# Performance work log

Measured on AMD Instinct MI355X. Metric: run time of the kernel, lower is better.

## Reference

```python
import jax, jax.numpy as jnp
import numpy as np

N, K, C, G = 100000, 16, 64, 8
EPS = 1e-5


def bn(x, gamma, beta):
    # training-mode BatchNorm1d over all dims except channel (last)
    axes = tuple(range(x.ndim - 1))
    m = jnp.mean(x, axis=axes)
    v = jnp.var(x, axis=axes)
    return (x - m) * jax.lax.rsqrt(v + EPS) * gamma + beta


def setup_inputs() -> dict:
    key = jax.random.key(0)
    ks = jax.random.split(key, 16)

    def lin(k, i, o):
        return (jax.random.normal(k, (i, o), jnp.float32) / np.sqrt(i)).astype(jnp.float32)

    feat = jax.random.normal(ks[0], (N, C), jnp.float32)
    coord = jax.random.uniform(ks[1], (N, 3), jnp.float32) * 10.0
    ref = jax.random.randint(ks[2], (N, K), 0, N)
    drop = jax.random.uniform(ks[3], (N, K)) < 0.05  # some padded (-1) neighbors
    ref = jnp.where(drop, -1, ref)

    return {
        "feat": feat, "coord": coord, "reference_index": ref,
        "wq": lin(ks[4], C, C), "bq": jnp.zeros((C,), jnp.float32),
        "gq": jnp.ones((C,), jnp.float32), "betaq": jnp.zeros((C,), jnp.float32),
        "wk": lin(ks[5], C, C), "bk": jnp.zeros((C,), jnp.float32),
        "gk": jnp.ones((C,), jnp.float32), "betak": jnp.zeros((C,), jnp.float32),
        "wv": lin(ks[6], C, C), "bv": jnp.zeros((C,), jnp.float32),
        "wp1": lin(ks[7], 3, C), "bp1": jnp.zeros((C,), jnp.float32),
        "gp": jnp.ones((C,), jnp.float32), "betap": jnp.zeros((C,), jnp.float32),
        "wp2": lin(ks[8], C, C), "bp2": jnp.zeros((C,), jnp.float32),
        "ww1": lin(ks[9], C, G), "bw1": jnp.zeros((G,), jnp.float32),
        "gw": jnp.ones((G,), jnp.float32), "betaw": jnp.zeros((G,), jnp.float32),
        "ww2": lin(ks[10], G, G), "bw2": jnp.zeros((G,), jnp.float32),
    }


def reference(feat, coord, reference_index,
              wq, bq, gq, betaq,
              wk, bk, gk, betak,
              wv, bv,
              wp1, bp1, gp, betap,
              wp2, bp2,
              ww1, bw1, gw, betaw,
              ww2, bw2):
    # q/k/v projections
    q = jax.nn.relu(bn(feat @ wq + bq, gq, betaq))   # [N, C]
    k = jax.nn.relu(bn(feat @ wk + bk, gk, betak))   # [N, C]
    v = feat @ wv + bv                                # [N, C]

    idx = jnp.clip(reference_index, 0, N - 1)         # clipped gather index [N, K]
    mask = (reference_index >= 0).astype(feat.dtype)  # sign(ref + 1)

    key_n = k[idx]                                    # [N, K, C] neighbor keys
    val = v[idx]                                      # [N, K, C]
    pos = coord[idx] - coord[:, None, :]              # [N, K, 3] relative coords

    relation_qk = key_n - q[:, None, :]               # [N, K, C]

    # pe_bias branch
    peb = jax.nn.relu(bn(pos @ wp1 + bp1, gp, betap)) @ wp2 + bp2  # [N, K, C]
    relation_qk = relation_qk + peb
    val = val + peb

    # weight encoding -> grouped softmax over neighbors, masked
    w = jax.nn.relu(bn(relation_qk @ ww1 + bw1, gw, betaw)) @ ww2 + bw2  # [N, K, G]
    w = jax.nn.softmax(w, axis=1) * mask[:, :, None]

    val = val.reshape(N, K, G, C // G)
    out = jnp.einsum('nsgi,nsg->ngi', val, w).reshape(N, C)
    return out
```

## Files before the change

### kernel.cpp

```cpp
#include <hip/hip_runtime.h>
#include <hip/hip_bf16.h>

#define NPTS 100000
#define KNBR 16
#define CCH  64
#define GRP  8
#define BN_EPS 1e-5f
#define NROW (NPTS * KNBR)
#define NBATCH (NROW / 64)
#define NPB   ((NPTS + 63) / 64)

#define O_QLINH 0
#define O_KLINH (NPTS * 32)
#define O_VLINH (NPTS * 64)
#define O_STAT  (NPTS * 96)
#define O_AFF   (O_STAT + 416)
#define O_W2W1  (O_AFF + 416)
#define O_BW1E  (O_W2W1 + 512)
#define O_QW1   (O_BW1E + 8)
#define O_KW1   (O_QW1 + NPTS * 8)

typedef __attribute__((ext_vector_type(8))) short short8;
typedef __attribute__((ext_vector_type(4))) short short4v;
typedef __attribute__((ext_vector_type(4))) float f32x4;
#define MFMA16(a, b, c) __builtin_amdgcn_mfma_f32_16x16x32_bf16(a, b, c, 0, 0, 0)

__device__ __forceinline__ int clip_idx(int r) {
    int i = r < 0 ? 0 : r;
    return i >= NPTS ? NPTS - 1 : i;
}
__device__ __forceinline__ unsigned short f2bf(float x) {
    union { float f; unsigned u; } v; v.f = x;
    unsigned r = v.u + 0x7fffu + ((v.u >> 16) & 1u);
    return (unsigned short)(r >> 16);
}
__device__ __forceinline__ float bf2f(unsigned short h) {
    union { unsigned u; float f; } v; v.u = ((unsigned)h) << 16;
    return v.f;
}
__device__ __forceinline__ int physK(int s) {
    return (s >> 5) * 32 + ((s >> 2) & 3) * 8 + ((s >> 4) & 1) * 4 + (s & 3);
}
__device__ __forceinline__ int aOff(int r, int p) {
    return r * 64 + (((p >> 3) ^ (r & 7)) << 3) + (p & 7);
}
__device__ __forceinline__ int kib_of(int i, int q) {
    return (i < 4) ? (4 * q + i) : (16 + 4 * q + (i - 4));
}

__global__ __launch_bounds__(512) void k_prep(
    const float* __restrict__ wp2, const float* __restrict__ ww1,
    const float* __restrict__ bw1, const float* __restrict__ bp2,
    float* __restrict__ stat, float* __restrict__ w2w1, float* __restrict__ bw1e)
{
    int t = threadIdx.x;
    if (t < 416) stat[t] = 0.f;
    int j = t >> 3, g = t & 7;
    float acc = 0.f;
    #pragma unroll 16
    for (int c = 0; c < 64; ++c) acc = fmaf(wp2[j * 64 + c], ww1[c * 8 + g], acc);
    w2w1[t] = acc;
    if (t < 8) {
        float b = bw1[t];
        #pragma unroll 16
        for (int c = 0; c < 64; ++c) b = fmaf(bp2[c], ww1[c * 8 + t], b);
        bw1e[t] = b;
    }
}

#define QKV_BLOCKS 512
__global__ __launch_bounds__(256) void k_qkv(
    const float* __restrict__ feat,
    const float* __restrict__ wq, const float* __restrict__ bq,
    const float* __restrict__ wk, const float* __restrict__ bk,
    const float* __restrict__ wv, const float* __restrict__ bv,
    const float* __restrict__ bp2,
    const float* __restrict__ coord, const int* __restrict__ ref,
    short* __restrict__ QlinH, short* __restrict__ KlinH, short* __restrict__ VlinH,
    float* __restrict__ stat)
{
    __shared__ short sA[4096];
    __shared__ float s_red[9];
    const int tid = threadIdx.x, lane = tid & 63, w = tid >> 6;
    const int q = lane >> 4, c15 = lane & 15;

    if (blockIdx.x >= QKV_BLOCKS) {
        float m[9];
        #pragma unroll
        for (int i = 0; i < 9; ++i) m[i] = 0.f;
        const int gid = (blockIdx.x - QKV_BLOCKS) * 256 + tid;
        const int stride = 128 * 256;
        for (int row = gid; row < NROW; row += stride) {
            int n = row >> 4;
            int idx = clip_idx(ref[row]);
            float px = coord[idx * 3 + 0] - coord[n * 3 + 0];
            float py = coord[idx * 3 + 1] - coord[n * 3 + 1];
            float pz = coord[idx * 3 + 2] - coord[n * 3 + 2];
            m[0] += px; m[1] += py; m[2] += pz;
            m[3] = fmaf(px, px, m[3]); m[4] = fmaf(py, py, m[4]); m[5] = fmaf(pz, pz, m[5]);
            m[6] = fmaf(px, py, m[6]); m[7] = fmaf(px, pz, m[7]); m[8] = fmaf(py, pz, m[8]);
        }
        if (tid < 9) s_red[tid] = 0.f;
        __syncthreads();
        #pragma unroll
        for (int off = 32; off >= 1; off >>= 1) {
            #pragma unroll
            for (int i = 0; i < 9; ++i) m[i] += __shfl_xor(m[i], off, 64);
        }
        if (lane == 0) {
            #pragma unroll
            for (int i = 0; i < 9; ++i) atomicAdd(&s_red[i], m[i]);
        }
        __syncthreads();
        if (tid < 9) atomicAdd(&stat[256 + tid], s_red[tid]);
        return;
    }

    short8 bfrag[3][2];
    float bias[3];
    #pragma unroll
    for (int t = 0; t < 3; ++t) {
        int gt = w * 3 + t;
        const float* W = (gt < 4) ? wq : (gt < 8) ? wk : wv;
        const float* B = (gt < 4) ? bq : (gt < 8) ? bk : bv;
        int col = (gt * 16 + c15) & 63;
        bias[t] = B[col] + (gt >= 8 ? bp2[col] : 0.f);
        #pragma unroll
        for (int kt = 0; kt < 2; ++kt) {
            short8 bb;
            #pragma unroll
            for (int i = 0; i < 8; ++i) {
                int kk = kt * 32 + kib_of(i, q);
                bb[i] = (short)f2bf(W[kk * 64 + col]);
            }
            bfrag[t][kt] = bb;
        }
    }
    float st_s[3], st_q[3];
    #pragma unroll
    for (int t = 0; t < 3; ++t) { st_s[t] = 0.f; st_q[t] = 0.f; }

    const int c4 = c15 * 4;
    const int pk4 = physK(c4);

    for (int b = blockIdx.x; b < NPB; b += QKV_BLOCKS) {
        const int pbase = b * 64;
        #pragma unroll
        for (int i = 0; i < 4; ++i) {
            int p = w * 16 + i * 4 + q;
            int n = pbase + p;
            float4 v = make_float4(0.f, 0.f, 0.f, 0.f);
            if (n < NPTS) v = *(const float4*)(feat + n * 64 + c4);
            short4v h;
            h[0] = (short)f2bf(v.x); h[1] = (short)f2bf(v.y);
            h[2] = (short)f2bf(v.z); h[3] = (short)f2bf(v.w);
            *(short4v*)(sA + aOff(p, pk4)) = h;
        }
        __syncthreads();
        #pragma unroll
        for (int mt = 0; mt < 4; ++mt) {
            int r = mt * 16 + c15;
            int ch0 = q ^ (r & 7);
            int ch1 = (4 + q) ^ (r & 7);
            short8 a0 = *(const short8*)(sA + r * 64 + (ch0 << 3));
            short8 a1 = *(const short8*)(sA + r * 64 + (ch1 << 3));
            #pragma unroll
            for (int t = 0; t < 3; ++t) {
                f32x4 acc = (f32x4){0.f, 0.f, 0.f, 0.f};
                acc = MFMA16(a0, bfrag[t][0], acc);
                acc = MFMA16(a1, bfrag[t][1], acc);
                int gt = w * 3 + t;
                #pragma unroll
                for (int rg = 0; rg < 4; ++rg) {
                    int row = mt * 16 + 4 * q + rg;
                    int n = pbase + row;
                    if (n < NPTS) {
                        unsigned short h = f2bf(acc[rg] + bias[t]);
                        float vr = bf2f(h);
                        if (gt < 4)      QlinH[n * 64 + gt * 16 + c15] = (short)h;
                        else if (gt < 8) KlinH[n * 64 + (gt - 4) * 16 + c15] = (short)h;
                        else             VlinH[n * 64 + (gt - 8) * 16 + c15] = (short)h;
                        if (gt < 8) { st_s[t] += vr; st_q[t] = fmaf(vr, vr, st_q[t]); }
                    }
                }
            }
        }
        __syncthreads();
    }
    #pragma unroll
    for (int t = 0; t < 3; ++t) {
        st_s[t] += __shfl_xor(st_s[t], 16, 64); st_s[t] += __shfl_xor(st_s[t], 32, 64);
        st_q[t] += __shfl_xor(st_q[t], 16, 64); st_q[t] += __shfl_xor(st_q[t], 32, 64);
    }
    if (q == 0) {
        #pragma unroll
        for (int t = 0; t < 3; ++t) {
            int gt = w * 3 + t;
            if (gt < 4) {
                atomicAdd(&stat[gt * 16 + c15], st_s[t]);
                atomicAdd(&stat[64 + gt * 16 + c15], st_q[t]);
            } else if (gt < 8) {
                atomicAdd(&stat[128 + (gt - 4) * 16 + c15], st_s[t]);
                atomicAdd(&stat[192 + (gt - 4) * 16 + c15], st_q[t]);
            }
        }
    }
}

__global__ __launch_bounds__(192) void k_finA(
    const float* __restrict__ gq, const float* __restrict__ betaq,
    const float* __restrict__ gk, const float* __restrict__ betak,
    const float* __restrict__ gp, const float* __restrict__ betap,
    const float* __restrict__ wp1, const float* __restrict__ bp1,
    const float* __restrict__ stat, float* __restrict__ aff)
{
    int t = threadIdx.x;
    if (t < 64) {
        float m = stat[t] / (float)NPTS;
        float v = stat[64 + t] / (float)NPTS - m * m;
        float a = gq[t] * rsqrtf(v + BN_EPS);
        aff[t] = a;
        aff[64 + t] = betaq[t] - m * a;
    } else if (t < 128) {
        int c = t - 64;
        float m = stat[128 + c] / (float)NPTS;
        float v = stat[192 + c] / (float)NPTS - m * m;
        float a = gk[c] * rsqrtf(v + BN_EPS);
        aff[128 + c] = a;
        aff[192 + c] = betak[c] - m * a;
    } else {
        int c = t - 128;
        const float R = (float)NROW;
        float Ex = stat[256] / R, Ey = stat[257] / R, Ez = stat[258] / R;
        float Exx = stat[259] / R, Eyy = stat[260] / R, Ezz = stat[261] / R;
        float Exy = stat[262] / R, Exz = stat[263] / R, Eyz = stat[264] / R;
        float Cxx = Exx - Ex * Ex, Cyy = Eyy - Ey * Ey, Czz = Ezz - Ez * Ez;
        float Cxy = Exy - Ex * Ey, Cxz = Exz - Ex * Ez, Cyz = Eyz - Ey * Ez;
        float a0 = wp1[c], a1 = wp1[64 + c], a2 = wp1[128 + c];
        float mean = a0 * Ex + a1 * Ey + a2 * Ez + bp1[c];
        float var = a0 * a0 * Cxx + a1 * a1 * Cyy + a2 * a2 * Czz
                  + 2.f * (a0 * a1 * Cxy + a0 * a2 * Cxz + a1 * a2 * Cyz);
        float a = gp[c] * rsqrtf(var + BN_EPS);
        aff[256 + c] = a;
        aff[320 + c] = betap[c] - mean * a;
    }
}

__global__ __launch_bounds__(128) void k_qkw(
    const short* __restrict__ QlinH, const short* __restrict__ KlinH,
    const float* __restrict__ ww1, const float* __restrict__ aff,
    float* __restrict__ QW1, float* __restrict__ KW1)
{
    __shared__ short sA[2][8192];
    const int tid = threadIdx.x, lane = tid & 63, w = tid >> 6;
    const int q = lane >> 4, g = lane & 15;
    short8 bimg[2];
    #pragma unroll
    for (int kt = 0; kt < 2; ++kt) {
        short8 bb;
        #pragma unroll
        for (int i = 0; i < 8; ++i) {
            int s = kt * 32 + kib_of(i, q);
            bb[i] = (short)f2bf(g < 8 ? ww1[s * 8 + g] : 0.f);
        }
        bimg[kt] = bb;
    }
    const int r8 = lane >> 3, c8 = (lane & 7) * 8;
    f32x4 qa0 = *(const f32x4*)(aff + c8),       qa1 = *(const f32x4*)(aff + c8 + 4);
    f32x4 qb0 = *(const f32x4*)(aff + 64 + c8),  qb1 = *(const f32x4*)(aff + 64 + c8 + 4);
    f32x4 ka0 = *(const f32x4*)(aff + 128 + c8), ka1 = *(const f32x4*)(aff + 128 + c8 + 4);
    f32x4 kb0 = *(const f32x4*)(aff + 192 + c8), kb1 = *(const f32x4*)(aff + 192 + c8 + 4);
    const int pkA = physK(c8), pkB = physK(c8 + 4);
    short* AQ = sA[w];
    short* AK = sA[w] + 4096;

    for (int b = blockIdx.x * 2 + w; b < NPB; b += gridDim.x * 2) {
        const int pbase = b * 64;
        #pragma unroll
        for (int it = 0; it < 8; ++it) {
            int p = it * 8 + r8;
            int n = pbase + p;
            short8 qraw = {0,0,0,0,0,0,0,0}, kraw = {0,0,0,0,0,0,0,0};
            if (n < NPTS) {
                qraw = *(const short8*)(QlinH + n * 64 + c8);
                kraw = *(const short8*)(KlinH + n * 64 + c8);
            }
            short4v qlo, qhi, klo, khi;
            #pragma unroll
            for (int e = 0; e < 4; ++e) {
                qlo[e] = (short)f2bf(fmaxf(fmaf(bf2f((unsigned short)qraw[e]), qa0[e], qb0[e]), 0.f));
                qhi[e] = (short)f2bf(fmaxf(fmaf(bf2f((unsigned short)qraw[e + 4]), qa1[e], qb1[e]), 0.f));
                klo[e] = (short)f2bf(fmaxf(fmaf(bf2f((unsigned short)kraw[e]), ka0[e], kb0[e]), 0.f));
                khi[e] = (short)f2bf(fmaxf(fmaf(bf2f((unsigned short)kraw[e + 4]), ka1[e], kb1[e]), 0.f));
            }
            *(short4v*)(AQ + aOff(p, pkA)) = qlo;
            *(short4v*)(AQ + aOff(p, pkB)) = qhi;
            *(short4v*)(AK + aOff(p, pkA)) = klo;
            *(short4v*)(AK + aOff(p, pkB)) = khi;
        }
        #pragma unroll
        for (int mt = 0; mt < 4; ++mt) {
            f32x4 aq = (f32x4){0.f, 0.f, 0.f, 0.f};
            f32x4 ak = (f32x4){0.f, 0.f, 0.f, 0.f};
            int r = mt * 16 + g;
            #pragma unroll
            for (int kt = 0; kt < 2; ++kt) {
                int chunk = (kt * 4 + q) ^ (r & 7);
                aq = MFMA16(*(const short8*)(AQ + r * 64 + (chunk << 3)), bimg[kt], aq);
                ak = MFMA16(*(const short8*)(AK + r * 64 + (chunk << 3)), bimg[kt], ak);
            }
            if (g < 8) {
                #pragma unroll
                for (int rg = 0; rg < 4; ++rg) {
                    int n = pbase + mt * 16 + 4 * q + rg;
                    if (n < NPTS) {
                        QW1[n * 8 + g] = aq[rg];
                        KW1[n * 8 + g] = ak[rg];
                    }
                }
            }
        }
    }
}

__global__ __launch_bounds__(128) void k_wstats(
    const float* __restrict__ coord, const int* __restrict__ ref,
    const float* __restrict__ wp1, const float* __restrict__ bp1,
    const float* __restrict__ bw1e, const float* __restrict__ w2w1,
    const float* __restrict__ QW1, const float* __restrict__ KW1,
    const float* __restrict__ aff, float* __restrict__ stat)
{
    __shared__ short sP[2][4096];
    __shared__ float sPos[2][256];
    __shared__ int   sIdx[2][64];
    __shared__ float sRed[16];
    const int tid = threadIdx.x, lane = tid & 63, w = tid >> 6;
    const int q = lane >> 4, g = lane & 15, g7 = lane & 7;
    short8 bimg[2];
    #pragma unroll
    for (int kt = 0; kt < 2; ++kt) {
        short8 bb;
        #pragma unroll
        for (int i = 0; i < 8; ++i) {
            int s = kt * 32 + kib_of(i, q);
            bb[i] = (short)f2bf(g < 8 ? w2w1[s * 8 + g] : 0.f);
        }
        bimg[kt] = bb;
    }
    if (tid < 16) sRed[tid] = 0.f;
    __syncthreads();

    const float pa = aff[256 + lane];
    const float A0 = pa * wp1[lane], A1 = pa * wp1[64 + lane], A2 = pa * wp1[128 + lane];
    const float B0 = fmaf(pa, bp1[lane], aff[320 + lane]);
    const float bwg = bw1e[g7];
    const int pk = physK(lane);

    short* P = sP[w];
    float* pos = sPos[w];
    int* idxs = sIdx[w];
    float accS = 0.f, accQ = 0.f;

    for (int b = blockIdx.x * 2 + w; b < NBATCH; b += gridDim.x * 2) {
        const int rbase = b * 64;
        const int p0 = b * 4;
        {
            int r = ref[rbase + lane];
            int idx = clip_idx(r);
            idxs[lane] = idx;
            int n = p0 + (lane >> 4);
            pos[lane * 4 + 0] = coord[idx * 3 + 0] - coord[n * 3 + 0];
            pos[lane * 4 + 1] = coord[idx * 3 + 1] - coord[n * 3 + 1];
            pos[lane * 4 + 2] = coord[idx * 3 + 2] - coord[n * 3 + 2];
        }
        float kwc[16], qwc[4];
        #pragma unroll
        for (int mt = 0; mt < 4; ++mt) {
            int4 i4 = *(const int4*)(idxs + mt * 16 + 4 * q);
            kwc[mt * 4 + 0] = KW1[i4.x * 8 + g7];
            kwc[mt * 4 + 1] = KW1[i4.y * 8 + g7];
            kwc[mt * 4 + 2] = KW1[i4.z * 8 + g7];
            kwc[mt * 4 + 3] = KW1[i4.w * 8 + g7];
            qwc[mt] = QW1[(p0 + mt) * 8 + g7];
        }
        #pragma unroll 8
        for (int rr = 0; rr < 64; ++rr) {
            f32x4 pp = *(const f32x4*)(pos + rr * 4);
            float p1v = fmaxf(fmaf(pp.x, A0, fmaf(pp.y, A1, fmaf(pp.z, A2, B0))), 0.f);
            P[aOff(rr, pk)] = (short)f2bf(p1v);
        }
        #pragma unroll
        for (int mt = 0; mt < 4; ++mt) {
            f32x4 acc = (f32x4){0.f, 0.f, 0.f, 0.f};
            int r = mt * 16 + g;
            #pragma unroll
            for (int kt = 0; kt < 2; ++kt) {
                int chunk = (kt * 4 + q) ^ (r & 7);
                acc = MFMA16(*(const short8*)(P + r * 64 + (chunk << 3)), bimg[kt], acc);
            }
            if (g < 8) {
                float dq = bwg - qwc[mt];
                #pragma unroll
                for (int rg = 0; rg < 4; ++rg) {
                    float W = acc[rg] + kwc[mt * 4 + rg] + dq;
                    accS += W;
                    accQ = fmaf(W, W, accQ);
                }
            }
        }
    }
    accS += __shfl_xor(accS, 16, 64); accS += __shfl_xor(accS, 32, 64);
    accQ += __shfl_xor(accQ, 16, 64); accQ += __shfl_xor(accQ, 32, 64);
    if (lane < 8) {
        atomicAdd(&sRed[lane], accS);
        atomicAdd(&sRed[8 + lane], accQ);
    }
    __syncthreads();
    if (tid < 16) atomicAdd(&stat[384 + tid], sRed[tid]);
}

__global__ __launch_bounds__(64) void k_finB(
    const float* __restrict__ gw_, const float* __restrict__ betaw,
    const float* __restrict__ stat, float* __restrict__ aff)
{
    int t = threadIdx.x;
    if (t < 8) {
        const float M = (float)NROW;
        float m = stat[384 + t] / M;
        float v = stat[392 + t] / M - m * m;
        float a = gw_[t] * rsqrtf(v + BN_EPS);
        aff[384 + t] = a;
        aff[392 + t] = betaw[t] - m * a;
    }
}

__global__ __launch_bounds__(128) void k_final(
    const float* __restrict__ coord, const int* __restrict__ ref,
    const float* __restrict__ wp1, const float* __restrict__ bp1,
    const float* __restrict__ wp2,
    const float* __restrict__ bw1e, const float* __restrict__ w2w1,
    const float* __restrict__ ww2, const float* __restrict__ bw2,
    const float* __restrict__ QW1, const float* __restrict__ KW1,
    const short* __restrict__ VlinH,
    const float* __restrict__ aff, float* __restrict__ out)
{
    __shared__ short sP[2][4096];
    __shared__ float sPos[2][256];
    __shared__ int   sIdx[2][64];
    __shared__ float sWn[2][576];
    __shared__ float sW2[72];
    const int tid = threadIdx.x, lane = tid & 63, w = tid >> 6;
    const int q = lane >> 4, g15 = lane & 15, g7 = lane & 7;

    if (tid < 64) sW2[tid] = ww2[tid];
    else if (tid < 72) sW2[tid] = bw2[tid - 64];
    __syncthreads();

    short8 bw_img[2];
    #pragma unroll
    for (int kt = 0; kt < 2; ++kt) {
        short8 bb;
        #pragma unroll
        for (int i = 0; i < 8; ++i) {
            int s = kt * 32 + kib_of(i, q);
            bb[i] = (short)f2bf(g15 < 8 ? w2w1[s * 8 + g15] : 0.f);
        }
        bw_img[kt] = bb;
    }
    short8 b1[8];
    #pragma unroll
    for (int tt = 0; tt < 8; ++tt) {
        int kt = tt & 1, nt = tt >> 1;
        short8 bb;
        #pragma unroll
        for (int i = 0; i < 8; ++i) {
            int kk = kt * 32 + kib_of(i, q);
            bb[i] = (short)f2bf(wp2[kk * 64 + nt * 16 + g15]);
        }
        b1[tt] = bb;
    }

    const float pa = aff[256 + lane];
    const float A0 = pa * wp1[lane], A1 = pa * wp1[64 + lane], A2 = pa * wp1[128 + lane];
    const float B0 = fmaf(pa, bp1[lane], aff[320 + lane]);
    const float bwg = bw1e[g7];
    const float wag = aff[384 + g7], wbg = aff[392 + g7];
    const int pk = physK(lane);

    short* P = sP[w];
    float* pos = sPos[w];
    int* idxs = sIdx[w];
    float* wn = sWn[w];

    for (int b = blockIdx.x * 2 + w; b < NBATCH; b += gridDim.x * 2) {
        const int rbase = b * 64;
        const int p0 = b * 4;
        {
            int r = ref[rbase + lane];
            int idx = clip_idx(r);
            idxs[lane] = idx;
            int n = p0 + (lane >> 4);
            pos[lane * 4 + 0] = coord[idx * 3 + 0] - coord[n * 3 + 0];
            pos[lane * 4 + 1] = coord[idx * 3 + 1] - coord[n * 3 + 1];
            pos[lane * 4 + 2] = coord[idx * 3 + 2] - coord[n * 3 + 2];
            pos[lane * 4 + 3] = (r >= 0) ? 1.f : 0.f;
        }
        float kwc[16], qwc[4];
        #pragma unroll
        for (int mt = 0; mt < 4; ++mt) {
            int4 i4 = *(const int4*)(idxs + mt * 16 + 4 * q);
            kwc[mt * 4 + 0] = KW1[i4.x * 8 + g7];
            kwc[mt * 4 + 1] = KW1[i4.y * 8 + g7];
            kwc[mt * 4 + 2] = KW1[i4.z * 8 + g7];
            kwc[mt * 4 + 3] = KW1[i4.w * 8 + g7];
            qwc[mt] = QW1[(p0 + mt) * 8 + g7];
        }
        #pragma unroll 8
        for (int rr = 0; rr < 64; ++rr) {
            f32x4 pp = *(const f32x4*)(pos + rr * 4);
            float p1v = fmaxf(fmaf(pp.x, A0, fmaf(pp.y, A1, fmaf(pp.z, A2, B0))), 0.f);
            P[aOff(rr, pk)] = (short)f2bf(p1v);
        }
        #pragma unroll
        for (int mt = 0; mt < 4; ++mt) {
            f32x4 acc = (f32x4){0.f, 0.f, 0.f, 0.f};
            int r = mt * 16 + g15;
            #pragma unroll
            for (int kt = 0; kt < 2; ++kt) {
                int chunk = (kt * 4 + q) ^ (r & 7);
                acc = MFMA16(*(const short8*)(P + r * 64 + (chunk << 3)), bw_img[kt], acc);
            }
            if (g15 < 8) {
                float dq = bwg - qwc[mt];
                #pragma unroll
                for (int rg = 0; rg < 4; ++rg) {
                    int row = mt * 16 + 4 * q + rg;
                    float W = acc[rg] + kwc[mt * 4 + rg] + dq;
                    wn[row * 9 + g15] = fmaxf(fmaf(wag, W, wbg), 0.f);
                }
            }
        }
        {
            float h[8];
            #pragma unroll
            for (int gg = 0; gg < 8; ++gg) h[gg] = wn[lane * 9 + gg];
            float mask = pos[lane * 4 + 3];
            #pragma unroll
            for (int o = 0; o < 8; ++o) {
                float acc = sW2[64 + o];
                #pragma unroll
                for (int gg = 0; gg < 8; ++gg) acc = fmaf(h[gg], sW2[gg * 8 + o], acc);
                float e = __expf(acc);
                float s = e;
                s += __shfl_xor(s, 1, 64);
                s += __shfl_xor(s, 2, 64);
                s += __shfl_xor(s, 4, 64);
                s += __shfl_xor(s, 8, 64);
                wn[lane * 9 + o] = e * __builtin_amdgcn_rcpf(s) * mask;
            }
        }
        #pragma unroll
        for (int mt = 0; mt < 4; ++mt) {
            int4 i4 = *(const int4*)(idxs + mt * 16 + 4 * q);
            int ia[4] = {i4.x, i4.y, i4.z, i4.w};
            unsigned short vc[16];
            #pragma unroll
            for (int rg = 0; rg < 4; ++rg) {
                const short* vb = VlinH + ia[rg] * 64 + g15;
                #pragma unroll
                for (int nt = 0; nt < 4; ++nt)
                    vc[rg * 4 + nt] = (unsigned short)vb[nt * 16];
            }
            int r = mt * 16 + g15;
            int c0 = q ^ (r & 7);
            int c1 = (4 + q) ^ (r & 7);
            short8 a0 = *(const short8*)(P + r * 64 + (c0 << 3));
            short8 a1 = *(const short8*)(P + r * 64 + (c1 << 3));
            const int ro0 = (mt * 16 + 4 * q) * 9;
            #pragma unroll
            for (int nt = 0; nt < 4; ++nt) {
                f32x4 acc = (f32x4){0.f, 0.f, 0.f, 0.f};
                acc = MFMA16(a0, b1[nt * 2 + 0], acc);
                acc = MFMA16(a1, b1[nt * 2 + 1], acc);
                int col = nt * 16 + g15;
                int o = nt * 2 + (g15 >> 3);
                float part = 0.f;
                #pragma unroll
                for (int rg = 0; rg < 4; ++rg) {
                    float v = bf2f(vc[rg * 4 + nt]);
                    part = fmaf(v + acc[rg], wn[ro0 + rg * 9 + o], part);
                }
                part += __shfl_xor(part, 16, 64);
                part += __shfl_xor(part, 32, 64);
                if (q == 0) out[(p0 + mt) * 64 + col] = part;
            }
        }
    }
}

extern "C" void kernel_launch(void* const* d_in, const int* in_sizes, int n_in,
                              void* d_out, int out_size, void* d_ws, size_t ws_size,
                              hipStream_t stream)
{
    const float* feat  = (const float*)d_in[0];
    const float* coord = (const float*)d_in[1];
    const int*   ref   = (const int*)d_in[2];
    const float* wq    = (const float*)d_in[3];
    const float* bq    = (const float*)d_in[4];
    const float* gq    = (const float*)d_in[5];
    const float* betaq = (const float*)d_in[6];
    const float* wk    = (const float*)d_in[7];
    const float* bk    = (const float*)d_in[8];
    const float* gk    = (const float*)d_in[9];
    const float* betak = (const float*)d_in[10];
    const float* wv    = (const float*)d_in[11];
    const float* bv    = (const float*)d_in[12];
    const float* wp1   = (const float*)d_in[13];
    const float* bp1   = (const float*)d_in[14];
    const float* gp    = (const float*)d_in[15];
    const float* betap = (const float*)d_in[16];
    const float* wp2   = (const float*)d_in[17];
    const float* bp2   = (const float*)d_in[18];
    const float* ww1   = (const float*)d_in[19];
    const float* bw1   = (const float*)d_in[20];
    const float* gw_   = (const float*)d_in[21];
    const float* betaw = (const float*)d_in[22];
    const float* ww2   = (const float*)d_in[23];
    const float* bw2   = (const float*)d_in[24];

    float* ws    = (float*)d_ws;
    short* QlinH = (short*)(ws + O_QLINH);
    short* KlinH = (short*)(ws + O_KLINH);
    short* VlinH = (short*)(ws + O_VLINH);
    float* stat  = ws + O_STAT;
    float* aff   = ws + O_AFF;
    float* w2w1  = ws + O_W2W1;
    float* bw1e  = ws + O_BW1E;
    float* QW1   = ws + O_QW1;
    float* KW1   = ws + O_KW1;
    float* out   = (float*)d_out;

    hipLaunchKernelGGL(k_prep, dim3(1), dim3(512), 0, stream,
                       wp2, ww1, bw1, bp2, stat, w2w1, bw1e);
    hipLaunchKernelGGL(k_qkv, dim3(QKV_BLOCKS + 128), dim3(256), 0, stream,
                       feat, wq, bq, wk, bk, wv, bv, bp2, coord, ref,
                       QlinH, KlinH, VlinH, stat);
    hipLaunchKernelGGL(k_finA, dim3(1), dim3(192), 0, stream,
                       gq, betaq, gk, betak, gp, betap, wp1, bp1, stat, aff);
    hipLaunchKernelGGL(k_qkw, dim3(782), dim3(128), 0, stream,
                       QlinH, KlinH, ww1, aff, QW1, KW1);
    hipLaunchKernelGGL(k_wstats, dim3(2500), dim3(128), 0, stream,
                       coord, ref, wp1, bp1, bw1e, w2w1, QW1, KW1, aff, stat);
    hipLaunchKernelGGL(k_finB, dim3(1), dim3(64), 0, stream, gw_, betaw, stat, aff);
    hipLaunchKernelGGL(k_final, dim3(2500), dim3(128), 0, stream,
                       coord, ref, wp1, bp1, wp2, bw1e, w2w1, ww2, bw2,
                       QW1, KW1, VlinH, aff, out);
}
```

Measured before the change: 263.6 us.

## Prefetch V gathers early and pack bf16 conversions with hardware cvt_pk

The V-neighbor gathers for all four row tiles are now issued ahead of time: two before the position MLP and two before the softmax. This hides global gather latency behind compute instead of stalling inside the einsum loop. Separately, manual bf16 rounding is replaced with the v_cvt_pk_bf16_f32 instruction, and each lane now computes two adjacent channels for half the rows, writing packed 32-bit LDS stores. The cost is higher register pressure from holding 64 prefetched values per lane, which may reduce occupancy.

```diff
diff --git a/kernel.cpp b/kernel.cpp
--- a/kernel.cpp
+++ b/kernel.cpp
@@ -37,6 +37,11 @@
 __device__ __forceinline__ float bf2f(unsigned short h) {
     union { unsigned u; float f; } v; v.u = ((unsigned)h) << 16;
     return v.f;
+}
+__device__ __forceinline__ unsigned pk_bf16(float lo, float hi) {
+    unsigned r;
+    asm("v_cvt_pk_bf16_f32 %0, %1, %2" : "=v"(r) : "v"(lo), "v"(hi));
+    return r;
 }
 __device__ __forceinline__ int physK(int s) {
     return (s >> 5) * 32 + ((s >> 2) & 3) * 8 + ((s >> 4) & 1) * 4 + (s & 3);
@@ -285,18 +290,22 @@
                 qraw = *(const short8*)(QlinH + n * 64 + c8);
                 kraw = *(const short8*)(KlinH + n * 64 + c8);
             }
-            short4v qlo, qhi, klo, khi;
+            float qf[8], kf[8];
             #pragma unroll
             for (int e = 0; e < 4; ++e) {
-                qlo[e] = (short)f2bf(fmaxf(fmaf(bf2f((unsigned short)qraw[e]), qa0[e], qb0[e]), 0.f));
-                qhi[e] = (short)f2bf(fmaxf(fmaf(bf2f((unsigned short)qraw[e + 4]), qa1[e], qb1[e]), 0.f));
-                klo[e] = (short)f2bf(fmaxf(fmaf(bf2f((unsigned short)kraw[e]), ka0[e], kb0[e]), 0.f));
-                khi[e] = (short)f2bf(fmaxf(fmaf(bf2f((unsigned short)kraw[e + 4]), ka1[e], kb1[e]), 0.f));
-            }
-            *(short4v*)(AQ + aOff(p, pkA)) = qlo;
-            *(short4v*)(AQ + aOff(p, pkB)) = qhi;
-            *(short4v*)(AK + aOff(p, pkA)) = klo;
-            *(short4v*)(AK + aOff(p, pkB)) = khi;
+                qf[e]     = fmaxf(fmaf(bf2f((unsigned short)qraw[e]), qa0[e], qb0[e]), 0.f);
+                qf[e + 4] = fmaxf(fmaf(bf2f((unsigned short)qraw[e + 4]), qa1[e], qb1[e]), 0.f);
+                kf[e]     = fmaxf(fmaf(bf2f((unsigned short)kraw[e]), ka0[e], kb0[e]), 0.f);
+                kf[e + 4] = fmaxf(fmaf(bf2f((unsigned short)kraw[e + 4]), ka1[e], kb1[e]), 0.f);
+            }
+            uint2 qv0 = make_uint2(pk_bf16(qf[0], qf[1]), pk_bf16(qf[2], qf[3]));
+            uint2 qv1 = make_uint2(pk_bf16(qf[4], qf[5]), pk_bf16(qf[6], qf[7]));
+            uint2 kv0 = make_uint2(pk_bf16(kf[0], kf[1]), pk_bf16(kf[2], kf[3]));
+            uint2 kv1 = make_uint2(pk_bf16(kf[4], kf[5]), pk_bf16(kf[6], kf[7]));
+            *(uint2*)(AQ + aOff(p, pkA)) = qv0;
+            *(uint2*)(AQ + aOff(p, pkB)) = qv1;
+            *(uint2*)(AK + aOff(p, pkA)) = kv0;
+            *(uint2*)(AK + aOff(p, pkB)) = kv1;
         }
         #pragma unroll
         for (int mt = 0; mt < 4; ++mt) {
@@ -350,11 +359,15 @@
     if (tid < 16) sRed[tid] = 0.f;
     __syncthreads();
 
-    const float pa = aff[256 + lane];
-    const float A0 = pa * wp1[lane], A1 = pa * wp1[64 + lane], A2 = pa * wp1[128 + lane];
-    const float B0 = fmaf(pa, bp1[lane], aff[320 + lane]);
+    const int c2 = (lane & 31) * 2, rh5 = (lane >> 5) * 32;
+    const float paL = aff[256 + c2],     paH = aff[256 + c2 + 1];
+    const float A0L = paL * wp1[c2],       A0H = paH * wp1[c2 + 1];
+    const float A1L = paL * wp1[64 + c2],  A1H = paH * wp1[64 + c2 + 1];
+    const float A2L = paL * wp1[128 + c2], A2H = paH * wp1[128 + c2 + 1];
+    const float B0L = fmaf(paL, bp1[c2], aff[320 + c2]);
+    const float B0H = fmaf(paH, bp1[c2 + 1], aff[320 + c2 + 1]);
+    const int pOff = physK(c2);
     const float bwg = bw1e[g7];
-    const int pk = physK(lane);
 
     short* P = sP[w];
     float* pos = sPos[w];
@@ -384,10 +397,12 @@
             qwc[mt] = QW1[(p0 + mt) * 8 + g7];
         }
         #pragma unroll 8
-        for (int rr = 0; rr < 64; ++rr) {
-            f32x4 pp = *(const f32x4*)(pos + rr * 4);
-            float p1v = fmaxf(fmaf(pp.x, A0, fmaf(pp.y, A1, fmaf(pp.z, A2, B0))), 0.f);
-            P[aOff(rr, pk)] = (short)f2bf(p1v);
+        for (int rr = 0; rr < 32; ++rr) {
+            int row = rh5 + rr;
+            f32x4 pp = *(const f32x4*)(pos + row * 4);
+            float lo = fmaxf(fmaf(pp.x, A0L, fmaf(pp.y, A1L, fmaf(pp.z, A2L, B0L))), 0.f);
+            float hi = fmaxf(fmaf(pp.x, A0H, fmaf(pp.y, A1H, fmaf(pp.z, A2H, B0H))), 0.f);
+            *(unsigned*)(P + aOff(row, pOff)) = pk_bf16(lo, hi);
         }
         #pragma unroll
         for (int mt = 0; mt < 4; ++mt) {
@@ -480,17 +495,59 @@
         b1[tt] = bb;
     }
 
-    const float pa = aff[256 + lane];
-    const float A0 = pa * wp1[lane], A1 = pa * wp1[64 + lane], A2 = pa * wp1[128 + lane];
-    const float B0 = fmaf(pa, bp1[lane], aff[320 + lane]);
+    const int c2 = (lane & 31) * 2, rh5 = (lane >> 5) * 32;
+    const float paL = aff[256 + c2],     paH = aff[256 + c2 + 1];
+    const float A0L = paL * wp1[c2],       A0H = paH * wp1[c2 + 1];
+    const float A1L = paL * wp1[64 + c2],  A1H = paH * wp1[64 + c2 + 1];
+    const float A2L = paL * wp1[128 + c2], A2H = paH * wp1[128 + c2 + 1];
+    const float B0L = fmaf(paL, bp1[c2], aff[320 + c2]);
+    const float B0H = fmaf(paH, bp1[c2 + 1], aff[320 + c2 + 1]);
+    const int pOff = physK(c2);
     const float bwg = bw1e[g7];
     const float wag = aff[384 + g7], wbg = aff[392 + g7];
-    const int pk = physK(lane);
 
     short* P = sP[w];
     float* pos = sPos[w];
     int* idxs = sIdx[w];
     float* wn = sWn[w];
+
+#define LOADV(MT, VC) do {                                              \
+        int4 i4_ = *(const int4*)(idxs + (MT) * 16 + 4 * q);            \
+        int ia_[4] = {i4_.x, i4_.y, i4_.z, i4_.w};                      \
+        _Pragma("unroll")                                               \
+        for (int rg = 0; rg < 4; ++rg) {                                \
+            const short* vb_ = VlinH + ia_[rg] * 64 + g15;              \
+            _Pragma("unroll")                                           \
+            for (int nt = 0; nt < 4; ++nt)                              \
+                VC[rg * 4 + nt] = (unsigned short)vb_[nt * 16];         \
+        }                                                               \
+    } while (0)
+
+#define EINSUM_MT(MT, VC) do {                                          \
+        int r_ = (MT) * 16 + g15;                                       \
+        int c0_ = q ^ (r_ & 7);                                         \
+        int c1_ = (4 + q) ^ (r_ & 7);                                   \
+        short8 a0_ = *(const short8*)(P + r_ * 64 + (c0_ << 3));        \
+        short8 a1_ = *(const short8*)(P + r_ * 64 + (c1_ << 3));        \
+        const int ro0_ = ((MT) * 16 + 4 * q) * 9;                       \
+        _Pragma("unroll")                                               \
+        for (int nt = 0; nt < 4; ++nt) {                                \
+            f32x4 acc_ = (f32x4){0.f, 0.f, 0.f, 0.f};                   \
+            acc_ = MFMA16(a0_, b1[nt * 2 + 0], acc_);                   \
+            acc_ = MFMA16(a1_, b1[nt * 2 + 1], acc_);                   \
+            int col_ = nt * 16 + g15;                                   \
+            int o_ = nt * 2 + (g15 >> 3);                               \
+            float part_ = 0.f;                                          \
+            _Pragma("unroll")                                           \
+            for (int rg = 0; rg < 4; ++rg) {                            \
+                float v_ = bf2f(VC[rg * 4 + nt]);                       \
+                part_ = fmaf(v_ + acc_[rg], wn[ro0_ + rg * 9 + o_], part_); \
+            }                                                           \
+            part_ += __shfl_xor(part_, 16, 64);                         \
+            part_ += __shfl_xor(part_, 32, 64);                         \
+            if (q == 0) out[(p0 + (MT)) * 64 + col_] = part_;           \
+        }                                                               \
+    } while (0)
 
     for (int b = blockIdx.x * 2 + w; b < NBATCH; b += gridDim.x * 2) {
         const int rbase = b * 64;
@@ -515,11 +572,16 @@
             kwc[mt * 4 + 3] = KW1[i4.w * 8 + g7];
             qwc[mt] = QW1[(p0 + mt) * 8 + g7];
         }
+        unsigned short vcA[16], vcB[16], vcC[16], vcD[16];
+        LOADV(0, vcA);
+        LOADV(1, vcB);
         #pragma unroll 8
-        for (int rr = 0; rr < 64; ++rr) {
-            f32x4 pp = *(const f32x4*)(pos + rr * 4);
-            float p1v = fmaxf(fmaf(pp.x, A0, fmaf(pp.y, A1, fmaf(pp.z, A2, B0))), 0.f);
-            P[aOff(rr, pk)] = (short)f2bf(p1v);
+        for (int rr = 0; rr < 32; ++rr) {
+            int row = rh5 + rr;
+            f32x4 pp = *(const f32x4*)(pos + row * 4);
+            float lo = fmaxf(fmaf(pp.x, A0L, fmaf(pp.y, A1L, fmaf(pp.z, A2L, B0L))), 0.f);
+            float hi = fmaxf(fmaf(pp.x, A0H, fmaf(pp.y, A1H, fmaf(pp.z, A2H, B0H))), 0.f);
+            *(unsigned*)(P + aOff(row, pOff)) = pk_bf16(lo, hi);
         }
         #pragma unroll
         for (int mt = 0; mt < 4; ++mt) {
@@ -540,6 +602,8 @@
                 }
             }
         }
+        LOADV(2, vcC);
+        LOADV(3, vcD);
         {
             float h[8];
             #pragma unroll
@@ -559,43 +623,13 @@
                 wn[lane * 9 + o] = e * __builtin_amdgcn_rcpf(s) * mask;
             }
         }
-        #pragma unroll
-        for (int mt = 0; mt < 4; ++mt) {
-            int4 i4 = *(const int4*)(idxs + mt * 16 + 4 * q);
-            int ia[4] = {i4.x, i4.y, i4.z, i4.w};
-            unsigned short vc[16];
-            #pragma unroll
-            for (int rg = 0; rg < 4; ++rg) {
-                const short* vb = VlinH + ia[rg] * 64 + g15;
-                #pragma unroll
-                for (int nt = 0; nt < 4; ++nt)
-                    vc[rg * 4 + nt] = (unsigned short)vb[nt * 16];
-            }
-            int r = mt * 16 + g15;
-            int c0 = q ^ (r & 7);
-            int c1 = (4 + q) ^ (r & 7);
-            short8 a0 = *(const short8*)(P + r * 64 + (c0 << 3));
-            short8 a1 = *(const short8*)(P + r * 64 + (c1 << 3));
-            const int ro0 = (mt * 16 + 4 * q) * 9;
-            #pragma unroll
-            for (int nt = 0; nt < 4; ++nt) {
-                f32x4 acc = (f32x4){0.f, 0.f, 0.f, 0.f};
-                acc = MFMA16(a0, b1[nt * 2 + 0], acc);
-                acc = MFMA16(a1, b1[nt * 2 + 1], acc);
-                int col = nt * 16 + g15;
-                int o = nt * 2 + (g15 >> 3);
-                float part = 0.f;
-                #pragma unroll
-                for (int rg = 0; rg < 4; ++rg) {
-                    float v = bf2f(vc[rg * 4 + nt]);
-                    part = fmaf(v + acc[rg], wn[ro0 + rg * 9 + o], part);
-                }
-                part += __shfl_xor(part, 16, 64);
-                part += __shfl_xor(part, 32, 64);
-                if (q == 0) out[(p0 + mt) * 64 + col] = part;
-            }
-        }
-    }
+        EINSUM_MT(0, vcA);
+        EINSUM_MT(1, vcB);
+        EINSUM_MT(2, vcC);
+        EINSUM_MT(3, vcD);
+    }
+#undef LOADV
+#undef EINSUM_MT
 }
 
 extern "C" void kernel_launch(void* const* d_in, const int* in_sizes, int n_in,
```

After: 220.7 us. -16.3%, faster.
